# Kernel tuning notes

Hardware: AMD Instinct MI355X
Metric: run time of the kernel (lower is better)

Reference implementation:

```python
import jax, jax.numpy as jnp
import numpy as np

PADDING_IDX = 0
SMOOTHING = 0.1


def setup_inputs() -> dict:
    key = jax.random.key(0)
    k1, k2 = jax.random.split(key)
    N, V = 4096, 32000
    # x plays the role of log-probabilities [N, V]
    x = jax.random.normal(k1, (N, V), dtype=jnp.float32)
    target = jax.random.randint(k2, (N,), 0, V, dtype=jnp.int64)
    return {"x": x, "target": target}


def reference(x, target):
    n = x.shape[-1]
    mask = (target != PADDING_IDX)  # [N] valid-token mask
    maskf = mask.astype(x.dtype)
    # smooth term: -sum over vocab of x, zeroed for padding rows, summed over batch
    loss = -jnp.sum(x * maskf[:, None])
    # nll term: gather log-prob at target class, ignore padding rows, sum
    gathered = jnp.take_along_axis(x, target[:, None], axis=1)[:, 0]  # [N]
    nll = -jnp.sum(gathered * maskf)
    return SMOOTHING * (loss / n) + (1.0 - SMOOTHING) * nll
```

## Files before the change

### kernel.cpp

```cpp
#include <hip/hip_runtime.h>


#define LS_V 32000
#define LS_V4 8000
#define LS_SMOOTH 0.1f

__global__ __launch_bounds__(256) void ls_row_reduce(
    const float* __restrict__ x,
    const int*   __restrict__ target,
    float*       __restrict__ out)
{
    const int row = blockIdx.x;
    const int tid = threadIdx.x;

    const int t = target[row];
    const bool valid = (t != 0);

    float s = 0.0f;
    if (valid) {
        const float4* __restrict__ xr =
            (const float4*)(x + (size_t)row * LS_V);
        for (int j = tid; j < LS_V4; j += 256) {
            float4 v = xr[j];
            s += (v.x + v.y) + (v.z + v.w);
        }
    }

    #pragma unroll
    for (int off = 32; off > 0; off >>= 1)
        s += __shfl_down(s, off, 64);

    __shared__ float wsum[4];
    const int lane = tid & 63;
    const int wave = tid >> 6;
    if (lane == 0) wsum[wave] = s;
    __syncthreads();

    if (tid == 0) {
        const float S = (wsum[0] + wsum[1]) + (wsum[2] + wsum[3]);
        const float g = valid ? x[(size_t)row * LS_V + t] : 0.0f;
        const float contrib = -(LS_SMOOTH / (float)LS_V) * S
                              - (1.0f - LS_SMOOTH) * g;
        atomicAdd(out, contrib);
    }
}

extern "C" void kernel_launch(void* const* d_in, const int* in_sizes, int n_in,
                              void* d_out, int out_size, void* d_ws, size_t ws_size,
                              hipStream_t stream)
{
    const float* x      = (const float*)d_in[0];
    const int*   target = (const int*)d_in[1];
    float*       out    = (float*)d_out;

    const int N = in_sizes[1];

    hipMemsetAsync(out, 0, sizeof(float), stream);

    ls_row_reduce<<<N, 256, 0, stream>>>(x, target, out);
}
```

Baseline: 676.9 us.

## Unroll row reduction with nontemporal loads and replace atomics with two-pass reduce

```diff
diff --git a/kernel.cpp b/kernel.cpp
--- a/kernel.cpp
+++ b/kernel.cpp
@@ -5,10 +5,12 @@
 #define LS_V4 8000
 #define LS_SMOOTH 0.1f
 
+typedef float f4 __attribute__((ext_vector_type(4)));
+
 __global__ __launch_bounds__(256) void ls_row_reduce(
     const float* __restrict__ x,
     const int*   __restrict__ target,
-    float*       __restrict__ out)
+    float*       __restrict__ partial)
 {
     const int row = blockIdx.x;
     const int tid = threadIdx.x;
@@ -16,33 +18,62 @@
     const int t = target[row];
     const bool valid = (t != 0);
 
-    float s = 0.0f;
+    float s0 = 0.0f, s1 = 0.0f;
     if (valid) {
-        const float4* __restrict__ xr =
-            (const float4*)(x + (size_t)row * LS_V);
-        for (int j = tid; j < LS_V4; j += 256) {
-            float4 v = xr[j];
-            s += (v.x + v.y) + (v.z + v.w);
+        const f4* __restrict__ xr =
+            (const f4*)(x + (size_t)row * LS_V);
+        int j = tid;
+        #pragma unroll 5
+        for (int i = 0; i < 15; ++i, j += 512) {
+            f4 a = __builtin_nontemporal_load(&xr[j]);
+            f4 b = __builtin_nontemporal_load(&xr[j + 256]);
+            s0 += (a.x + a.y) + (a.z + a.w);
+            s1 += (b.x + b.y) + (b.z + b.w);
+        }
+        {
+            f4 a = __builtin_nontemporal_load(&xr[j]);
+            s0 += (a.x + a.y) + (a.z + a.w);
+            if (tid < 64) {
+                f4 b = __builtin_nontemporal_load(&xr[j + 256]);
+                s1 += (b.x + b.y) + (b.z + b.w);
+            }
         }
     }
+
+    float s = s0 + s1;
+    #pragma unroll
+    for (int off = 32; off > 0; off >>= 1)
+        s += __shfl_down(s, off, 64);
+
+    __shared__ float wsum[4];
+    if ((tid & 63) == 0) wsum[tid >> 6] = s;
+    __syncthreads();
+
+    if (tid == 0) {
+        const float S = (wsum[0] + wsum[1]) + (wsum[2] + wsum[3]);
+        const float g = valid ? x[(size_t)row * LS_V + t] : 0.0f;
+        partial[row] = -(LS_SMOOTH / (float)LS_V) * S
+                       - (1.0f - LS_SMOOTH) * g;
+    }
+}
+
+__global__ __launch_bounds__(256) void ls_final(
+    const float* __restrict__ partial,
+    float*       __restrict__ out,
+    int n)
+{
+    const int tid = threadIdx.x;
+    float s = 0.0f;
+    for (int i = tid; i < n; i += 256) s += partial[i];
 
     #pragma unroll
     for (int off = 32; off > 0; off >>= 1)
         s += __shfl_down(s, off, 64);
 
     __shared__ float wsum[4];
-    const int lane = tid & 63;
-    const int wave = tid >> 6;
-    if (lane == 0) wsum[wave] = s;
+    if ((tid & 63) == 0) wsum[tid >> 6] = s;
     __syncthreads();
-
-    if (tid == 0) {
-        const float S = (wsum[0] + wsum[1]) + (wsum[2] + wsum[3]);
-        const float g = valid ? x[(size_t)row * LS_V + t] : 0.0f;
-        const float contrib = -(LS_SMOOTH / (float)LS_V) * S
-                              - (1.0f - LS_SMOOTH) * g;
-        atomicAdd(out, contrib);
-    }
+    if (tid == 0) out[0] = (wsum[0] + wsum[1]) + (wsum[2] + wsum[3]);
 }
 
 extern "C" void kernel_launch(void* const* d_in, const int* in_sizes, int n_in,
@@ -52,10 +83,10 @@
     const float* x      = (const float*)d_in[0];
     const int*   target = (const int*)d_in[1];
     float*       out    = (float*)d_out;
+    float*       part   = (float*)d_ws;
 
     const int N = in_sizes[1];
 
-    hipMemsetAsync(out, 0, sizeof(float), stream);
-
-    ls_row_reduce<<<N, 256, 0, stream>>>(x, target, out);
+    ls_row_reduce<<<N, 256, 0, stream>>>(x, target, part);
+    ls_final<<<1, 256, 0, stream>>>(part, out, N);
 }
```

Result: faster. 628.8 us (-7.1%).
